# Performance work log

Measured on AMD Instinct MI355X. Metric: run time of the kernel, lower is better.

Reference implementation:

```python
import jax, jax.numpy as jnp
import numpy as np

B, T, HID = 2, 2048, 2048
NH, NKV, HD = 32, 8, 64


def setup_inputs() -> dict:
    key = jax.random.key(0)
    ks = jax.random.split(key, 5)
    x = jax.random.normal(ks[0], (B, T, HID), dtype=jnp.float32)
    position_ids = jnp.broadcast_to(jnp.arange(T, dtype=jnp.int32), (B, T))
    s = 0.02
    Wq = jax.random.normal(ks[1], (NH * HD, HID), dtype=jnp.float32) * s
    Wk = jax.random.normal(ks[2], (NKV * HD, HID), dtype=jnp.float32) * s
    Wv = jax.random.normal(ks[3], (NKV * HD, HID), dtype=jnp.float32) * s
    Wo = jax.random.normal(ks[4], (HID, NH * HD), dtype=jnp.float32) * s
    return {"x": x, "position_ids": position_ids, "Wq": Wq, "Wk": Wk, "Wv": Wv, "Wo": Wo}


def _rotate_half(t):
    t1, t2 = jnp.split(t, 2, axis=-1)
    return jnp.concatenate([-t2, t1], axis=-1)


def reference(x, position_ids, Wq, Wk, Wv, Wo):
    Bd, Td, _ = x.shape
    q = (x @ Wq.T).reshape(Bd, Td, NH, HD)
    k = (x @ Wk.T).reshape(Bd, Td, NKV, HD)
    v = (x @ Wv.T).reshape(Bd, Td, NKV, HD)

    # DummyRotaryEmbedding: freqs over even indices, repeat_interleave(2)
    freqs = 1.0 / (10000.0 ** (jnp.arange(0, HD, 2, dtype=jnp.float32) / HD))
    angles = position_ids.astype(jnp.float32)[:, :, None] * freqs  # [B,T,HD/2]
    cos = jnp.repeat(jnp.cos(angles), 2, axis=-1)[:, :, None, :]   # [B,T,1,HD]
    sin = jnp.repeat(jnp.sin(angles), 2, axis=-1)[:, :, None, :]

    q = q * cos + _rotate_half(q) * sin
    k = k * cos + _rotate_half(k) * sin

    n_rep = NH // NKV
    k = jnp.repeat(k, n_rep, axis=2)  # [B,T,NH,HD]
    v = jnp.repeat(v, n_rep, axis=2)

    scale = 1.0 / np.sqrt(HD).astype(np.float32)
    scores = jnp.einsum('bqhd,bkhd->bhqk', q, k) * scale  # [B,NH,T,T]
    probs = jax.nn.softmax(scores, axis=-1)
    out = jnp.einsum('bhqk,bkhd->bqhd', probs, v).reshape(Bd, Td, NH * HD)
    return out @ Wo.T
```

## Files before the change

kernel.cpp:

```cpp
#include <hip/hip_runtime.h>
#include <hip/hip_bf16.h>
#include <stdint.h>


typedef __attribute__((ext_vector_type(8))) short short8;
typedef __attribute__((ext_vector_type(4))) float f32x4;
typedef __attribute__((ext_vector_type(16))) float f32x16;

__device__ __forceinline__ unsigned short f2bf(float f) {
  union { float f; uint32_t u; } x; x.f = f;
  uint32_t r = x.u + 0x7fffu + ((x.u >> 16) & 1u);
  return (unsigned short)(r >> 16);
}
__device__ __forceinline__ float bf2f(unsigned short u) {
  union { uint32_t u; float f; } x; x.u = ((uint32_t)u) << 16;
  return x.f;
}
__device__ __forceinline__ uint32_t cvt_pk_bf16(float a, float b) {
  uint32_t r;
  asm("v_cvt_pk_bf16_f32 %0, %1, %2" : "=v"(r) : "v"(a), "v"(b));
  return r;
}
__device__ __forceinline__ void pl32swap(uint32_t& dst, uint32_t& src) {
  asm("v_permlane32_swap_b32 %0, %1" : "+v"(dst), "+v"(src));
}

__device__ __forceinline__ void gload_lds16(const void* g, void* l) {
  __builtin_amdgcn_global_load_lds(
      (const __attribute__((address_space(1))) unsigned int*)g,
      (__attribute__((address_space(3))) unsigned int*)l, 16, 0, 0);
}

#define VMCNT(n) asm volatile("s_waitcnt vmcnt(" #n ")" ::: "memory")
#define LGKMCNT0 asm volatile("s_waitcnt lgkmcnt(0)" ::: "memory")

__global__ __launch_bounds__(256) void convert_kernel(
    const float* __restrict__ x, const float* __restrict__ Wq,
    const float* __restrict__ Wk, const float* __restrict__ Wv,
    const float* __restrict__ Wo,
    unsigned short* __restrict__ xb, unsigned short* __restrict__ wqkvb,
    unsigned short* __restrict__ wob) {
  const int NX = 2097152;
  const int NQ = 1048576;
  const int NK = 262144;
  const int NV = 262144;
  const int NO = 1048576;
  const int total = NX + NQ + NK + NV + NO;
  for (int i = blockIdx.x * blockDim.x + threadIdx.x; i < total;
       i += gridDim.x * blockDim.x) {
    const float4* s; unsigned short* d; int o;
    if (i < NX)                 { o = i;               s = (const float4*)x;  d = xb; }
    else if (i < NX+NQ)         { o = i-NX;            s = (const float4*)Wq; d = wqkvb; }
    else if (i < NX+NQ+NK)      { o = i-NX-NQ;         s = (const float4*)Wk; d = wqkvb + 4194304; }
    else if (i < NX+NQ+NK+NV)   { o = i-NX-NQ-NK;      s = (const float4*)Wv; d = wqkvb + 5242880; }
    else                        { o = i-NX-NQ-NK-NV;   s = (const float4*)Wo; d = wob; }
    float4 v = s[o];
    ushort4 r;
    r.x = f2bf(v.x); r.y = f2bf(v.y); r.z = f2bf(v.z); r.w = f2bf(v.w);
    *(ushort4*)(d + (size_t)o * 4) = r;
  }
}

template <int NQ, typename OutT>
__global__ __launch_bounds__(512, 2) void gemm_2cu(
    const unsigned short* __restrict__ A, const unsigned short* __restrict__ Bt,
    OutT* __restrict__ C, int N, int K) {
  __shared__ unsigned short lA[2][128 * 64];
  __shared__ unsigned short lB[2][NQ * 64 * 64];
  const int tid  = threadIdx.x;
  const int lane = tid & 63;
  const int w    = tid >> 6;
  const int wr   = w >> 2, wc = w & 3;
  const long tm  = (long)blockIdx.y * 128;
  const long tn  = (long)blockIdx.x * (NQ * 64);

  f32x4 acc[4][NQ];
#pragma unroll
  for (int fi = 0; fi < 4; ++fi)
#pragma unroll
    for (int nq = 0; nq < NQ; ++nq) acc[fi][nq] = (f32x4){0.f, 0.f, 0.f, 0.f};

  const int srow = tid >> 3;
  const int sgr  = ((tid & 7) ^ (srow & 7)) * 8;
  const unsigned short* ga = A  + (tm + srow) * (long)K + sgr;
  const unsigned short* gb = Bt + (tn + srow) * (long)K + sgr;

  int aoff[4][2], boff[NQ][2];
#pragma unroll
  for (int fi = 0; fi < 4; ++fi)
#pragma unroll
    for (int ks = 0; ks < 2; ++ks) {
      int gk = (lane >> 4) + ks * 4;
      aoff[fi][ks] = (wr * 64 + fi * 16 + (lane & 15)) * 128 + ((gk ^ (lane & 7)) << 4);
    }
#pragma unroll
  for (int nq = 0; nq < NQ; ++nq)
#pragma unroll
    for (int ks = 0; ks < 2; ++ks) {
      int gk = (lane >> 4) + ks * 4;
      boff[nq][ks] = (wc * (NQ * 16) + nq * 16 + (lane & 15)) * 128 + ((gk ^ (lane & 7)) << 4);
    }

#pragma unroll
  for (int i = 0; i < 2; ++i)  gload_lds16(ga + (long)(64 * i) * K, &lA[0][tid * 8 + 4096 * i]);
#pragma unroll
  for (int i = 0; i < NQ; ++i) gload_lds16(gb + (long)(64 * i) * K, &lB[0][tid * 8 + 4096 * i]);
  VMCNT(0);
  __builtin_amdgcn_s_barrier();

  const int nk = K >> 6;
  for (int t = 0; t < nk; ++t) {
    const int slot = t & 1;
    const unsigned short* gaT = ga + (long)((t + 1) << 6);
    const unsigned short* gbT = gb + (long)((t + 1) << 6);
    const bool st = (t + 1 < nk);
    const char* As = (const char*)lA[slot];
    const char* Bs = (const char*)lB[slot];
    unsigned short* dA = &lA[slot ^ 1][tid * 8];
    unsigned short* dB = &lB[slot ^ 1][tid * 8];

    short8 af[4][2];
#pragma unroll
    for (int nq = 0; nq < NQ; ++nq) {
      if (nq == 0) {
#pragma unroll
        for (int fi = 0; fi < 4; ++fi)
#pragma unroll
          for (int ks = 0; ks < 2; ++ks)
            af[fi][ks] = *(const short8*)(As + aoff[fi][ks]);
      }
      short8 bf0 = *(const short8*)(Bs + boff[nq][0]);
      short8 bf1 = *(const short8*)(Bs + boff[nq][1]);
      if (st && nq == 0) {
        gload_lds16(gaT,                 dA);
        gload_lds16(gaT + (long)64 * K,  dA + 4096);
#pragma unroll
        for (int i = 0; i < NQ; ++i)
          gload_lds16(gbT + (long)(64 * i) * K, dB + 4096 * i);
      }
      __builtin_amdgcn_s_barrier();
      LGKMCNT0;
      __builtin_amdgcn_sched_barrier(0);
      __builtin_amdgcn_s_setprio(1);
#pragma unroll
      for (int fi = 0; fi < 4; ++fi)
        acc[fi][nq] = __builtin_amdgcn_mfma_f32_16x16x32_bf16(af[fi][0], bf0, acc[fi][nq], 0, 0, 0);
#pragma unroll
      for (int fi = 0; fi < 4; ++fi)
        acc[fi][nq] = __builtin_amdgcn_mfma_f32_16x16x32_bf16(af[fi][1], bf1, acc[fi][nq], 0, 0, 0);
      __builtin_amdgcn_s_setprio(0);
      __builtin_amdgcn_sched_barrier(0);
      if (nq == NQ - 1) VMCNT(0);
      __builtin_amdgcn_s_barrier();
    }
  }

#pragma unroll
  for (int fi = 0; fi < 4; ++fi)
#pragma unroll
    for (int nq = 0; nq < NQ; ++nq) {
      long col = tn + wc * (NQ * 16) + nq * 16 + (lane & 15);
#pragma unroll
      for (int i = 0; i < 4; ++i) {
        long row = tm + wr * 64 + fi * 16 + (lane >> 4) * 4 + i;
        float v = acc[fi][nq][i];
        if constexpr (sizeof(OutT) == 2) C[row * N + col] = (OutT)f2bf(v);
        else                             C[row * N + col] = (OutT)v;
      }
    }
}

__global__ __launch_bounds__(256) void rope_kernel(
    unsigned short* __restrict__ qkv, const int* __restrict__ pos_ids,
    unsigned short* __restrict__ Vt) {
  const int m = blockIdx.x;
  const int b = m >> 11, t = m & 2047;
  const int tid = threadIdx.x;
  const float QSCALE = 0.18033688011112042f;
  __shared__ float cs[32], sn[32];
  if (tid < 32) {
    float pos = (float)pos_ids[m];
    float a = pos * exp2f(-(float)tid * 0.4152410118609203f);
    float s_, c_;
    sincosf(a, &s_, &c_);
    cs[tid] = c_; sn[tid] = s_;
  }
  __syncthreads();
  unsigned short* row = qkv + (size_t)m * 3072;

  const int qc = tid * 8;
  short8 qa = *(const short8*)(row + qc);
  short8 qp = *(const short8*)(row + (qc ^ 32));
  short8 ka = {}, kp = {};
  if (tid < 64) {
    const int kc = 2048 + tid * 8;
    ka = *(const short8*)(row + kc);
    kp = *(const short8*)(row + (kc ^ 32));
  }
  __syncthreads();

  {
    const int dbase = qc & 63;
    const float sgn = (qc & 32) ? 1.0f : -1.0f;
    short8 out;
#pragma unroll
    for (int j = 0; j < 8; ++j) {
      int fi = (dbase + j) >> 1;
      float o = bf2f((unsigned short)qa[j]) * cs[fi] +
                sgn * bf2f((unsigned short)qp[j]) * sn[fi];
      out[j] = (short)f2bf(o * QSCALE);
    }
    *(short8*)(row + qc) = out;
  }
  if (tid < 64) {
    const int kc = 2048 + tid * 8;
    const int dbase = (tid * 8) & 63;
    const float sgn = ((tid * 8) & 32) ? 1.0f : -1.0f;
    short8 out;
#pragma unroll
    for (int j = 0; j < 8; ++j) {
      int fi = (dbase + j) >> 1;
      float o = bf2f((unsigned short)ka[j]) * cs[fi] +
                sgn * bf2f((unsigned short)kp[j]) * sn[fi];
      out[j] = (short)f2bf(o);
    }
    *(short8*)(row + kc) = out;
  }
  {
    int e = tid * 2;
    unsigned short v0 = row[2560 + e];
    unsigned short v1 = row[2560 + e + 1];
    int g = e >> 6, d = e & 63;
    unsigned short* vt = Vt + ((size_t)((b * 8 + g) * 64 + d)) * 2048 + t;
    vt[0] = v0;
    vt[2048] = v1;
  }
}

__global__ __launch_bounds__(512) void attn_kernel(
    const unsigned short* __restrict__ qkv,
    const unsigned short* __restrict__ Vt,
    unsigned short* __restrict__ attnout) {
  const int qt = blockIdx.x, g = blockIdx.y, b = blockIdx.z;
  const int tid = threadIdx.x, lane = tid & 63, w = tid >> 6;
  const int l31 = lane & 31, hi = lane >> 5;
  const int h = g * 4 + (w & 3);
  const int qbase = qt * 64 + (w >> 2) * 32;

  __shared__ unsigned short lK[2][64 * 64];
  __shared__ unsigned short lV[3][64 * 64];

  short8 qf[4];
  {
    const unsigned short* qrow =
        qkv + ((size_t)(b * 2048 + qbase + l31)) * 3072 + h * 64 + hi * 8;
#pragma unroll
    for (int kc = 0; kc < 4; ++kc) qf[kc] = *(const short8*)(qrow + kc * 16);
  }

  f32x16 o0, o1;
#pragma unroll
  for (int i = 0; i < 16; ++i) { o0[i] = 0.f; o1[i] = 0.f; }
  float lrun = 0.f;

  const unsigned short* kgbase = qkv + (size_t)b * 2048 * 3072 + 2048 + g * 64;
  const unsigned short* vgbase = Vt + ((size_t)(b * 8 + g) * 64) * 2048;
  const int srow = w * 8 + (lane >> 3);
  const int sg = ((lane & 7) ^ (srow & 7)) * 8;

  int koff[2][4];
#pragma unroll
  for (int s = 0; s < 2; ++s)
#pragma unroll
    for (int kc = 0; kc < 4; ++kc) {
      int r = s * 32 + l31;
      koff[s][kc] = r * 128 + (((kc * 2 + hi) ^ (r & 7)) << 4);
    }

#define STAGE(kbuf, vbuf, kb)                                                       \
  {                                                                                 \
    const unsigned short* kk_ = kgbase + (size_t)((kb) * 64) * 3072;                \
    const unsigned short* vv_ = vgbase + (kb) * 64;                                 \
    gload_lds16(kk_ + (size_t)srow * 3072 + sg, &lK[kbuf][(w * 8) * 64]);           \
    gload_lds16(vv_ + (size_t)srow * 2048 + sg, &lV[vbuf][(w * 8) * 64]);           \
  }

#define PV_BLOCK(VBASE)                                                             \
  {                                                                                 \
    const char* Vb_ = (VBASE);                                                      \
    _Pragma("unroll")                                                               \
    for (int ks = 0; ks < 2; ++ks) {                                                \
      union { uint32_t u[4]; short8 s8; } fa, fb;                                   \
      _Pragma("unroll")                                                             \
      for (int u = 0; u < 4; ++u) { fa.u[u] = wd[ks][u]; fb.u[u] = wd[ks][4 + u]; } \
      const int kk0 = ks * 2, kk1 = ks * 2 + 1;                                     \
      short8 va0 = *(const short8*)(Vb_ + koff[0][kk0]);                            \
      short8 va1 = *(const short8*)(Vb_ + koff[1][kk0]);                            \
      o0 = __builtin_amdgcn_mfma_f32_32x32x16_bf16(fa.s8, va0, o0, 0, 0, 0);        \
      o1 = __builtin_amdgcn_mfma_f32_32x32x16_bf16(fa.s8, va1, o1, 0, 0, 0);        \
      short8 vb0 = *(const short8*)(Vb_ + koff[0][kk1]);                            \
      short8 vb1 = *(const short8*)(Vb_ + koff[1][kk1]);                            \
      o0 = __builtin_amdgcn_mfma_f32_32x32x16_bf16(fb.s8, vb0, o0, 0, 0, 0);        \
      o1 = __builtin_amdgcn_mfma_f32_32x32x16_bf16(fb.s8, vb1, o1, 0, 0, 0);        \
    }                                                                               \
  }

  uint32_t wd[2][8];

  STAGE(0, 0, 0);
  __syncthreads();

  int vnext = 1;
#pragma unroll 1
  for (int t = 0; t < 32; ++t) {
    if (t + 1 < 32) STAGE((t + 1) & 1, vnext, t + 1);
    const char* Kb = (const char*)lK[t & 1];
    const int vprev = (vnext == 2) ? 0 : vnext + 1;

    f32x16 s0, s1;
#pragma unroll
    for (int i = 0; i < 16; ++i) { s0[i] = 0.f; s1[i] = 0.f; }
    __builtin_amdgcn_s_setprio(1);
#pragma unroll
    for (int kc = 0; kc < 4; ++kc) {
      short8 k0 = *(const short8*)(Kb + koff[0][kc]);
      short8 k1 = *(const short8*)(Kb + koff[1][kc]);
      s0 = __builtin_amdgcn_mfma_f32_32x32x16_bf16(k0, qf[kc], s0, 0, 0, 0);
      s1 = __builtin_amdgcn_mfma_f32_32x32x16_bf16(k1, qf[kc], s1, 0, 0, 0);
    }
    if (t > 0) PV_BLOCK((const char*)lV[vprev]);
    __builtin_amdgcn_s_setprio(0);

#pragma unroll
    for (int i = 0; i < 16; ++i) { s0[i] = __builtin_amdgcn_exp2f(s0[i]); lrun += s0[i]; }
#pragma unroll
    for (int i = 0; i < 16; ++i) { s1[i] = __builtin_amdgcn_exp2f(s1[i]); lrun += s1[i]; }

#pragma unroll
    for (int mi = 0; mi < 8; ++mi) {
      wd[0][mi] = cvt_pk_bf16(s0[2 * mi], s0[2 * mi + 1]);
      wd[1][mi] = cvt_pk_bf16(s1[2 * mi], s1[2 * mi + 1]);
    }
#pragma unroll
    for (int ks = 0; ks < 2; ++ks) {
      pl32swap(wd[ks][0], wd[ks][2]);
      pl32swap(wd[ks][1], wd[ks][3]);
      pl32swap(wd[ks][4], wd[ks][6]);
      pl32swap(wd[ks][5], wd[ks][7]);
    }

    vnext = (vnext == 2) ? 0 : vnext + 1;
    __syncthreads();
  }

  PV_BLOCK((const char*)lV[1]);

  lrun += __shfl_xor(lrun, 32);
  float inv = 1.0f / lrun;
  const size_t obase =
      (size_t)(b * 2048 + qbase) * 2048 + h * 64 + l31;
#pragma unroll
  for (int reg = 0; reg < 16; ++reg) {
    int q = (reg & 3) + 8 * (reg >> 2) + 4 * hi;
    float invq = __shfl(inv, q);
    attnout[obase + (size_t)q * 2048]      = f2bf(o0[reg] * invq);
    attnout[obase + (size_t)q * 2048 + 32] = f2bf(o1[reg] * invq);
  }
#undef STAGE
#undef PV_BLOCK
}

extern "C" void kernel_launch(void* const* d_in, const int* in_sizes, int n_in,
                              void* d_out, int out_size, void* d_ws, size_t ws_size,
                              hipStream_t stream) {
  (void)in_sizes; (void)n_in; (void)out_size; (void)ws_size;
  const float* x  = (const float*)d_in[0];
  const int* pos  = (const int*)d_in[1];
  const float* Wq = (const float*)d_in[2];
  const float* Wk = (const float*)d_in[3];
  const float* Wv = (const float*)d_in[4];
  const float* Wo = (const float*)d_in[5];
  float* out = (float*)d_out;
  char* ws = (char*)d_ws;

  unsigned short* xb      = (unsigned short*)(ws);
  unsigned short* wqkvb   = (unsigned short*)(ws + 16777216);
  unsigned short* wob     = (unsigned short*)(ws + 29360128);
  unsigned short* qkv     = (unsigned short*)(ws + 37748736);
  unsigned short* Vt      = (unsigned short*)(ws + 62914560);
  unsigned short* attnout = (unsigned short*)(ws + 67108864);

  convert_kernel<<<2048, 256, 0, stream>>>(x, Wq, Wk, Wv, Wo, xb, wqkvb, wob);
  gemm_2cu<3, unsigned short><<<dim3(16, 32), 512, 0, stream>>>(xb, wqkvb, qkv, 3072, 2048);
  rope_kernel<<<4096, 256, 0, stream>>>(qkv, pos, Vt);
  attn_kernel<<<dim3(32, 8, 2), 512, 0, stream>>>(qkv, Vt, attnout);
  gemm_2cu<2, float><<<dim3(16, 32), 512, 0, stream>>>(attnout, wob, out, 2048, 2048);
}
```

Measured before the change: 202.0 us.

## Compute softmax row sums with MFMA and widen conversion and V buffering

The attention kernel now accumulates the softmax denominator with an extra MFMA that multiplies the bf16 probabilities by a ones vector. This replaces the per-lane VALU adds and the cross-lane shuffles in the epilogue, at the cost of four more MFMAs per key tile. The V LDS ring grows to four buffers, indexed directly by tile number, and the main loop is unrolled by four. The first QK MFMA now takes a zero accumulator instead of an explicit clear. The fp32-to-bf16 convert kernel also handles eight elements per thread with 16-byte stores.

Result: slower. 207.1 us (+2.5%).

```diff
diff --git a/kernel.cpp b/kernel.cpp
--- a/kernel.cpp
+++ b/kernel.cpp
@@ -40,11 +40,11 @@
     const float* __restrict__ Wo,
     unsigned short* __restrict__ xb, unsigned short* __restrict__ wqkvb,
     unsigned short* __restrict__ wob) {
-  const int NX = 2097152;
-  const int NQ = 1048576;
-  const int NK = 262144;
-  const int NV = 262144;
-  const int NO = 1048576;
+  const int NX = 1048576;
+  const int NQ = 524288;
+  const int NK = 131072;
+  const int NV = 131072;
+  const int NO = 524288;
   const int total = NX + NQ + NK + NV + NO;
   for (int i = blockIdx.x * blockDim.x + threadIdx.x; i < total;
        i += gridDim.x * blockDim.x) {
@@ -54,10 +54,14 @@
     else if (i < NX+NQ+NK)      { o = i-NX-NQ;         s = (const float4*)Wk; d = wqkvb + 4194304; }
     else if (i < NX+NQ+NK+NV)   { o = i-NX-NQ-NK;      s = (const float4*)Wv; d = wqkvb + 5242880; }
     else                        { o = i-NX-NQ-NK-NV;   s = (const float4*)Wo; d = wob; }
-    float4 v = s[o];
-    ushort4 r;
-    r.x = f2bf(v.x); r.y = f2bf(v.y); r.z = f2bf(v.z); r.w = f2bf(v.w);
-    *(ushort4*)(d + (size_t)o * 4) = r;
+    float4 v0 = s[(size_t)o * 2];
+    float4 v1 = s[(size_t)o * 2 + 1];
+    short8 r;
+    r[0] = (short)f2bf(v0.x); r[1] = (short)f2bf(v0.y);
+    r[2] = (short)f2bf(v0.z); r[3] = (short)f2bf(v0.w);
+    r[4] = (short)f2bf(v1.x); r[5] = (short)f2bf(v1.y);
+    r[6] = (short)f2bf(v1.z); r[7] = (short)f2bf(v1.w);
+    *(short8*)(d + (size_t)o * 8) = r;
   }
 }
 
@@ -248,7 +252,7 @@
   const int qbase = qt * 64 + (w >> 2) * 32;
 
   __shared__ unsigned short lK[2][64 * 64];
-  __shared__ unsigned short lV[3][64 * 64];
+  __shared__ unsigned short lV[4][64 * 64];
 
   short8 qf[4];
   {
@@ -258,10 +262,12 @@
     for (int kc = 0; kc < 4; ++kc) qf[kc] = *(const short8*)(qrow + kc * 16);
   }
 
-  f32x16 o0, o1;
-#pragma unroll
-  for (int i = 0; i < 16; ++i) { o0[i] = 0.f; o1[i] = 0.f; }
-  float lrun = 0.f;
+  f32x16 o0, o1, lacc, zro;
+#pragma unroll
+  for (int i = 0; i < 16; ++i) { o0[i] = 0.f; o1[i] = 0.f; lacc[i] = 0.f; zro[i] = 0.f; }
+
+  const short8 ones = {(short)0x3F80, (short)0x3F80, (short)0x3F80, (short)0x3F80,
+                       (short)0x3F80, (short)0x3F80, (short)0x3F80, (short)0x3F80};
 
   const unsigned short* kgbase = qkv + (size_t)b * 2048 * 3072 + 2048 + g * 64;
   const unsigned short* vgbase = Vt + ((size_t)(b * 8 + g) * 64) * 2048;
@@ -277,12 +283,12 @@
       koff[s][kc] = r * 128 + (((kc * 2 + hi) ^ (r & 7)) << 4);
     }
 
-#define STAGE(kbuf, vbuf, kb)                                                       \
+#define STAGE(kb)                                                                   \
   {                                                                                 \
     const unsigned short* kk_ = kgbase + (size_t)((kb) * 64) * 3072;                \
     const unsigned short* vv_ = vgbase + (kb) * 64;                                 \
-    gload_lds16(kk_ + (size_t)srow * 3072 + sg, &lK[kbuf][(w * 8) * 64]);           \
-    gload_lds16(vv_ + (size_t)srow * 2048 + sg, &lV[vbuf][(w * 8) * 64]);           \
+    gload_lds16(kk_ + (size_t)srow * 3072 + sg, &lK[(kb) & 1][(w * 8) * 64]);       \
+    gload_lds16(vv_ + (size_t)srow * 2048 + sg, &lV[(kb) & 3][(w * 8) * 64]);       \
   }
 
 #define PV_BLOCK(VBASE)                                                             \
@@ -290,81 +296,80 @@
     const char* Vb_ = (VBASE);                                                      \
     _Pragma("unroll")                                                               \
     for (int ks = 0; ks < 2; ++ks) {                                                \
-      union { uint32_t u[4]; short8 s8; } fa, fb;                                   \
-      _Pragma("unroll")                                                             \
-      for (int u = 0; u < 4; ++u) { fa.u[u] = wd[ks][u]; fb.u[u] = wd[ks][4 + u]; } \
       const int kk0 = ks * 2, kk1 = ks * 2 + 1;                                     \
       short8 va0 = *(const short8*)(Vb_ + koff[0][kk0]);                            \
       short8 va1 = *(const short8*)(Vb_ + koff[1][kk0]);                            \
-      o0 = __builtin_amdgcn_mfma_f32_32x32x16_bf16(fa.s8, va0, o0, 0, 0, 0);        \
-      o1 = __builtin_amdgcn_mfma_f32_32x32x16_bf16(fa.s8, va1, o1, 0, 0, 0);        \
+      o0   = __builtin_amdgcn_mfma_f32_32x32x16_bf16(wd[ks].s8[0], va0, o0, 0, 0, 0);  \
+      o1   = __builtin_amdgcn_mfma_f32_32x32x16_bf16(wd[ks].s8[0], va1, o1, 0, 0, 0);  \
+      lacc = __builtin_amdgcn_mfma_f32_32x32x16_bf16(wd[ks].s8[0], ones, lacc, 0, 0, 0);\
       short8 vb0 = *(const short8*)(Vb_ + koff[0][kk1]);                            \
       short8 vb1 = *(const short8*)(Vb_ + koff[1][kk1]);                            \
-      o0 = __builtin_amdgcn_mfma_f32_32x32x16_bf16(fb.s8, vb0, o0, 0, 0, 0);        \
-      o1 = __builtin_amdgcn_mfma_f32_32x32x16_bf16(fb.s8, vb1, o1, 0, 0, 0);        \
+      o0   = __builtin_amdgcn_mfma_f32_32x32x16_bf16(wd[ks].s8[1], vb0, o0, 0, 0, 0);  \
+      o1   = __builtin_amdgcn_mfma_f32_32x32x16_bf16(wd[ks].s8[1], vb1, o1, 0, 0, 0);  \
+      lacc = __builtin_amdgcn_mfma_f32_32x32x16_bf16(wd[ks].s8[1], ones, lacc, 0, 0, 0);\
     }                                                                               \
   }
 
-  uint32_t wd[2][8];
-
-  STAGE(0, 0, 0);
+  union PW { uint32_t u[8]; short8 s8[2]; };
+  PW wd[2];
+
+  STAGE(0);
   __syncthreads();
 
-  int vnext = 1;
-#pragma unroll 1
+#pragma unroll 4
   for (int t = 0; t < 32; ++t) {
-    if (t + 1 < 32) STAGE((t + 1) & 1, vnext, t + 1);
+    if (t + 1 < 32) STAGE(t + 1);
     const char* Kb = (const char*)lK[t & 1];
-    const int vprev = (vnext == 2) ? 0 : vnext + 1;
 
     f32x16 s0, s1;
-#pragma unroll
-    for (int i = 0; i < 16; ++i) { s0[i] = 0.f; s1[i] = 0.f; }
     __builtin_amdgcn_s_setprio(1);
-#pragma unroll
-    for (int kc = 0; kc < 4; ++kc) {
+    {
+      short8 k0 = *(const short8*)(Kb + koff[0][0]);
+      short8 k1 = *(const short8*)(Kb + koff[1][0]);
+      s0 = __builtin_amdgcn_mfma_f32_32x32x16_bf16(k0, qf[0], zro, 0, 0, 0);
+      s1 = __builtin_amdgcn_mfma_f32_32x32x16_bf16(k1, qf[0], zro, 0, 0, 0);
+    }
+#pragma unroll
+    for (int kc = 1; kc < 4; ++kc) {
       short8 k0 = *(const short8*)(Kb + koff[0][kc]);
       short8 k1 = *(const short8*)(Kb + koff[1][kc]);
       s0 = __builtin_amdgcn_mfma_f32_32x32x16_bf16(k0, qf[kc], s0, 0, 0, 0);
       s1 = __builtin_amdgcn_mfma_f32_32x32x16_bf16(k1, qf[kc], s1, 0, 0, 0);
     }
-    if (t > 0) PV_BLOCK((const char*)lV[vprev]);
+    if (t > 0) PV_BLOCK((const char*)lV[(t - 1) & 3]);
     __builtin_amdgcn_s_setprio(0);
 
 #pragma unroll
-    for (int i = 0; i < 16; ++i) { s0[i] = __builtin_amdgcn_exp2f(s0[i]); lrun += s0[i]; }
-#pragma unroll
-    for (int i = 0; i < 16; ++i) { s1[i] = __builtin_amdgcn_exp2f(s1[i]); lrun += s1[i]; }
+    for (int i = 0; i < 16; ++i) s0[i] = __builtin_amdgcn_exp2f(s0[i]);
+#pragma unroll
+    for (int i = 0; i < 16; ++i) s1[i] = __builtin_amdgcn_exp2f(s1[i]);
 
 #pragma unroll
     for (int mi = 0; mi < 8; ++mi) {
-      wd[0][mi] = cvt_pk_bf16(s0[2 * mi], s0[2 * mi + 1]);
-      wd[1][mi] = cvt_pk_bf16(s1[2 * mi], s1[2 * mi + 1]);
+      wd[0].u[mi] = cvt_pk_bf16(s0[2 * mi], s0[2 * mi + 1]);
+      wd[1].u[mi] = cvt_pk_bf16(s1[2 * mi], s1[2 * mi + 1]);
     }
 #pragma unroll
     for (int ks = 0; ks < 2; ++ks) {
-      pl32swap(wd[ks][0], wd[ks][2]);
-      pl32swap(wd[ks][1], wd[ks][3]);
-      pl32swap(wd[ks][4], wd[ks][6]);
-      pl32swap(wd[ks][5], wd[ks][7]);
-    }
-
-    vnext = (vnext == 2) ? 0 : vnext + 1;
+      pl32swap(wd[ks].u[0], wd[ks].u[2]);
+      pl32swap(wd[ks].u[1], wd[ks].u[3]);
+      pl32swap(wd[ks].u[4], wd[ks].u[6]);
+      pl32swap(wd[ks].u[5], wd[ks].u[7]);
+    }
+
     __syncthreads();
   }
 
-  PV_BLOCK((const char*)lV[1]);
-
-  lrun += __shfl_xor(lrun, 32);
-  float inv = 1.0f / lrun;
+  PV_BLOCK((const char*)lV[3]);
+
   const size_t obase =
       (size_t)(b * 2048 + qbase) * 2048 + h * 64 + l31;
 #pragma unroll
   for (int reg = 0; reg < 16; ++reg) {
     int q = (reg & 3) + 8 * (reg >> 2) + 4 * hi;
-    float invq = __shfl(inv, q);
-    attnout[obase + (size_t)q * 2048]      = f2bf(o0[reg] * invq);
-    attnout[obase + (size_t)q * 2048 + 32] = f2bf(o1[reg] * invq);
+    float inv = __builtin_amdgcn_rcpf(lacc[reg]);
+    attnout[obase + (size_t)q * 2048]      = f2bf(o0[reg] * inv);
+    attnout[obase + (size_t)q * 2048 + 32] = f2bf(o1[reg] * inv);
   }
 #undef STAGE
 #undef PV_BLOCK
```
